# Performance work log

Measured on AMD Instinct MI355X. Metric: run time of the kernel, lower is better.

The kernel has to match this reference:

```python
import jax, jax.numpy as jnp
import numpy as np

D_MODEL = 1024
NUM_EXPERTS = 64
TOP_K = 2
TEMPERATURE = 1.0


def setup_inputs() -> dict:
    key = jax.random.key(0)
    k1, k2, k3, k4 = jax.random.split(key, 4)
    mh_output = jax.random.normal(k1, (8, 4096, D_MODEL), dtype=jnp.float32)
    noise = jax.random.normal(k2, (8, 4096, NUM_EXPERTS), dtype=jnp.float32)  # randn_like sample, externalized
    # nn.Linear weights: shape [out, in], init normal(0, 0.02); biases zero
    W_route = jax.random.normal(k3, (NUM_EXPERTS, D_MODEL), dtype=jnp.float32) * 0.02
    b_route = jnp.zeros((NUM_EXPERTS,), dtype=jnp.float32)
    W_noise = jax.random.normal(k4, (NUM_EXPERTS, D_MODEL), dtype=jnp.float32) * 0.02
    b_noise = jnp.zeros((NUM_EXPERTS,), dtype=jnp.float32)
    return {"mh_output": mh_output, "noise": noise, "W_route": W_route,
            "b_route": b_route, "W_noise": W_noise, "b_noise": b_noise}


def reference(mh_output, noise, W_route, b_route, W_noise, b_noise):
    # logits = topkroute_linear(mh_output); noise_logits = noise_linear(mh_output)
    logits = jnp.einsum('bsd,ed->bse', mh_output, W_route) + b_route
    noise_logits = jnp.einsum('bsd,ed->bse', mh_output, W_noise) + b_noise
    # noisy logits = logits + temperature * randn * softplus(noise_logits)
    noisy = logits + TEMPERATURE * noise * jax.nn.softplus(noise_logits)
    # top-k, scatter into -inf, softmax  ==  softmax over top-k values scattered into zeros
    top_vals, indices = jax.lax.top_k(noisy, TOP_K)          # [b, s, k]
    probs_k = jax.nn.softmax(top_vals, axis=-1)              # softmax(-inf elsewhere) -> 0 elsewhere
    one_hot = jax.nn.one_hot(indices, NUM_EXPERTS, dtype=noisy.dtype)  # [b, s, k, E]
    router_output = jnp.sum(one_hot * probs_k[..., None], axis=-2)     # [b, s, E]
    return router_output, indices
```

## Files before the change

kernel.cpp:

```cpp
#include <hip/hip_runtime.h>
#include <math.h>


#define T_TOKENS 32768
#define D_MODEL  1024
#define NE       64
#define NCOL     128
#define M_TILE   64
#define KB       32
#define NCHUNK   (D_MODEL / KB)
#define CS_LD    65
#define OUT_IDX_BASE ((size_t)T_TOKENS * NE)
#define W_ELEMS  (NCOL * D_MODEL)

typedef short  bf16x8  __attribute__((ext_vector_type(8)));
typedef float  floatx4 __attribute__((ext_vector_type(4)));

__device__ __forceinline__ unsigned short f32_to_bf16_rne(float x) {
    unsigned u = __float_as_uint(x);
    unsigned r = u + 0x7fffu + ((u >> 16) & 1u);
    return (unsigned short)(r >> 16);
}
__device__ __forceinline__ float bf16_bits_to_f32(unsigned short h) {
    return __uint_as_float(((unsigned)h) << 16);
}
__device__ __forceinline__ int4 pack8(const unsigned short* h) {
    int4 r;
    r.x = (int)((unsigned)h[0] | ((unsigned)h[1] << 16));
    r.y = (int)((unsigned)h[2] | ((unsigned)h[3] << 16));
    r.z = (int)((unsigned)h[4] | ((unsigned)h[5] << 16));
    r.w = (int)((unsigned)h[6] | ((unsigned)h[7] << 16));
    return r;
}
__device__ __forceinline__ float softplus_f(float x) {
    return fmaxf(x, 0.f) + log1pf(expf(-fabsf(x)));
}

__global__ __launch_bounds__(256) void prepack_w(
    const float* __restrict__ Wr, const float* __restrict__ Wn,
    short* __restrict__ Bh, short* __restrict__ Bl)
{
    int g   = blockIdx.x * 256 + threadIdx.x;
    int n   = g & 15;
    int kg  = (g >> 4) & 127;
    int t2  = g >> 11;
    int col = t2 * 16 + n;
    const float* src = (col < NE ? Wr + (size_t)col * D_MODEL
                                 : Wn + (size_t)(col - NE) * D_MODEL) + kg * 8;
    float4 a = *(const float4*)src;
    float4 b = *(const float4*)(src + 4);
    float v[8] = {a.x, a.y, a.z, a.w, b.x, b.y, b.z, b.w};
    unsigned short h[8], l[8];
    #pragma unroll
    for (int j = 0; j < 8; ++j) {
        h[j] = f32_to_bf16_rne(v[j]);
        l[j] = f32_to_bf16_rne(v[j] - bf16_bits_to_f32(h[j]));
    }
    *(int4*)(Bh + (size_t)g * 8) = pack8(h);
    *(int4*)(Bl + (size_t)g * 8) = pack8(l);
}

__global__ __launch_bounds__(256) void router_mfma(
    const float* __restrict__ A,
    const float* __restrict__ noise,
    const float* __restrict__ br,
    const float* __restrict__ bn,
    const short* __restrict__ Bh,
    const short* __restrict__ Bl,
    float* __restrict__ out)
{
    __shared__ __align__(16) short Ah[2][M_TILE * KB];
    __shared__ __align__(16) short Al[2][M_TILE * KB];
    __shared__ float Cs[NCOL * CS_LD];
    __shared__ float s_p1[M_TILE], s_p2[M_TILE];
    __shared__ int   s_e1[M_TILE], s_e2[M_TILE];

    const int tid  = threadIdx.x;
    const int lane = tid & 63;
    const int wid  = tid >> 6;
    const int wm   = wid & 1;
    const int wn   = wid >> 1;
    const int n16  = lane & 15;
    const int quad = lane >> 4;
    const int m0   = blockIdx.x * M_TILE;

    const int ms = tid & 63;
    const int ks = tid >> 6;
    const float* pA = A + (size_t)(m0 + ms) * D_MODEL + ks * 8;
    const int sgbase = (ks * 64 + ms) * 8;

    const int bLaneOff = (quad * 16 + n16) * 8;
    const size_t bWaveBase = (size_t)(wn * 4) * 16384 + bLaneOff;

    floatx4 acc[2][4];
    #pragma unroll
    for (int i = 0; i < 2; ++i)
        #pragma unroll
        for (int j = 0; j < 4; ++j) acc[i][j] = (floatx4)0.f;

    float4 g0 = *(const float4*)pA;
    float4 g1 = *(const float4*)(pA + 4);
    {
        float v[8] = {g0.x, g0.y, g0.z, g0.w, g1.x, g1.y, g1.z, g1.w};
        unsigned short h[8], l[8];
        #pragma unroll
        for (int j = 0; j < 8; ++j) {
            h[j] = f32_to_bf16_rne(v[j]);
            l[j] = f32_to_bf16_rne(v[j] - bf16_bits_to_f32(h[j]));
        }
        *(int4*)&Ah[0][sgbase] = pack8(h);
        *(int4*)&Al[0][sgbase] = pack8(l);
    }
    bf16x8 bhc[4], blc[4];
    #pragma unroll
    for (int nf = 0; nf < 4; ++nf) {
        size_t o = bWaveBase + (size_t)nf * 16384;
        bhc[nf] = *(const bf16x8*)(Bh + o);
        blc[nf] = *(const bf16x8*)(Bl + o);
    }

    for (int kc = 0; kc < NCHUNK; ++kc) {
        const int cur = kc & 1, nxt = cur ^ 1;
        __syncthreads();

        float4 n0, n1;
        if (kc + 1 < NCHUNK) {
            n0 = *(const float4*)(pA + (kc + 1) * KB);
            n1 = *(const float4*)(pA + (kc + 1) * KB + 4);
        }

        bf16x8 afh[2], afl[2];
        #pragma unroll
        for (int mf = 0; mf < 2; ++mf) {
            int g = (quad * 64 + wm * 32 + mf * 16 + n16) * 8;
            afh[mf] = *(const bf16x8*)&Ah[cur][g];
            afl[mf] = *(const bf16x8*)&Al[cur][g];
        }

        bf16x8 bhn[4], bln[4];
        if (kc + 1 < NCHUNK) {
            #pragma unroll
            for (int nf = 0; nf < 4; ++nf) {
                size_t o = bWaveBase + (size_t)nf * 16384 + (size_t)(kc + 1) * 512;
                bhn[nf] = *(const bf16x8*)(Bh + o);
                bln[nf] = *(const bf16x8*)(Bl + o);
            }
        }

        #pragma unroll
        for (int mf = 0; mf < 2; ++mf)
            #pragma unroll
            for (int nf = 0; nf < 4; ++nf) {
                acc[mf][nf] = __builtin_amdgcn_mfma_f32_16x16x32_bf16(afh[mf], bhc[nf], acc[mf][nf], 0, 0, 0);
                acc[mf][nf] = __builtin_amdgcn_mfma_f32_16x16x32_bf16(afh[mf], blc[nf], acc[mf][nf], 0, 0, 0);
                acc[mf][nf] = __builtin_amdgcn_mfma_f32_16x16x32_bf16(afl[mf], bhc[nf], acc[mf][nf], 0, 0, 0);
            }

        if (kc + 1 < NCHUNK) {
            float v[8] = {n0.x, n0.y, n0.z, n0.w, n1.x, n1.y, n1.z, n1.w};
            unsigned short h[8], l[8];
            #pragma unroll
            for (int j = 0; j < 8; ++j) {
                h[j] = f32_to_bf16_rne(v[j]);
                l[j] = f32_to_bf16_rne(v[j] - bf16_bits_to_f32(h[j]));
            }
            *(int4*)&Ah[nxt][sgbase] = pack8(h);
            *(int4*)&Al[nxt][sgbase] = pack8(l);
            #pragma unroll
            for (int nf = 0; nf < 4; ++nf) { bhc[nf] = bhn[nf]; blc[nf] = bln[nf]; }
        }
    }

    #pragma unroll
    for (int mf = 0; mf < 2; ++mf)
        #pragma unroll
        for (int nf = 0; nf < 4; ++nf) {
            int col = wn * 64 + nf * 16 + n16;
            int tb  = wm * 32 + mf * 16 + quad * 4;
            #pragma unroll
            for (int r = 0; r < 4; ++r)
                Cs[col * CS_LD + tb + r] = acc[mf][nf][r];
        }
    __syncthreads();

    {
        const int e  = tid & 63;
        const int th = tid >> 6;
        float brv = br[e], bnv = bn[e];
        #pragma unroll
        for (int j = 0; j < 16; ++j) {
            int t = th * 16 + j;
            float route = Cs[e * CS_LD + t] + brv;
            float nl    = Cs[(e + NE) * CS_LD + t] + bnv;
            float nz    = noise[(size_t)(m0 + t) * NE + e];
            Cs[e * CS_LD + t] = fmaf(nz, softplus_f(nl), route);
        }
    }
    __syncthreads();

    if (tid < M_TILE) {
        const int t = tid;
        float v1 = -INFINITY, v2 = -INFINITY;
        int e1 = 0, e2 = 0;
        #pragma unroll 8
        for (int e = 0; e < NE; ++e) {
            float v = Cs[e * CS_LD + t];
            if (v > v1) { v2 = v1; e2 = e1; v1 = v; e1 = e; }
            else if (v > v2) { v2 = v; e2 = e; }
        }
        float ex = expf(v2 - v1);
        float denom = 1.f + ex;
        s_p1[t] = 1.f / denom;
        s_p2[t] = ex / denom;
        s_e1[t] = e1;
        s_e2[t] = e2;
        float2 iv = make_float2((float)e1, (float)e2);
        *(float2*)(out + OUT_IDX_BASE + (size_t)(m0 + t) * 2) = iv;
    }
    __syncthreads();

    #pragma unroll
    for (int i = 0; i < 4; ++i) {
        int gi = i * 256 + tid;
        int t  = gi >> 4;
        int e0 = (gi & 15) * 4;
        float p1 = s_p1[t], p2 = s_p2[t];
        int   e1 = s_e1[t], e2 = s_e2[t];
        float4 v;
        v.x = (e0 + 0 == e1) ? p1 : ((e0 + 0 == e2) ? p2 : 0.f);
        v.y = (e0 + 1 == e1) ? p1 : ((e0 + 1 == e2) ? p2 : 0.f);
        v.z = (e0 + 2 == e1) ? p1 : ((e0 + 2 == e2) ? p2 : 0.f);
        v.w = (e0 + 3 == e1) ? p1 : ((e0 + 3 == e2) ? p2 : 0.f);
        *(float4*)(out + (size_t)(m0 + t) * NE + e0) = v;
    }
}

extern "C" void kernel_launch(void* const* d_in, const int* in_sizes, int n_in,
                              void* d_out, int out_size, void* d_ws, size_t ws_size,
                              hipStream_t stream) {
    const float* A     = (const float*)d_in[0];
    const float* noise = (const float*)d_in[1];
    const float* Wr    = (const float*)d_in[2];
    const float* br    = (const float*)d_in[3];
    const float* Wn    = (const float*)d_in[4];
    const float* bn    = (const float*)d_in[5];
    float* out = (float*)d_out;

    short* Bh = (short*)d_ws;
    short* Bl = Bh + W_ELEMS;

    prepack_w<<<dim3(W_ELEMS / 8 / 256), dim3(256), 0, stream>>>(Wr, Wn, Bh, Bl);
    router_mfma<<<dim3(T_TOKENS / M_TILE), dim3(256), 0, stream>>>(A, noise, br, bn, Bh, Bl, out);
}
```

Measured before the change: 235.6 us.

## Drop LDS staging for A and pair route/noise columns per wave for register epilogue

Each wave now loads its own A rows straight from global memory into registers, converts them to bf16 hi/lo there, and feeds them to MFMA. This removes the LDS double buffer and the per-chunk __syncthreads, and adds a two-deep register prefetch of A. The token tile shrinks to 32 with 4 blocks/SM launch bounds to raise occupancy. Each wave's N-fragments are chosen so it holds both the route and the noise columns for the same experts, so softplus and the bias can be applied from accumulators without a full C staging pass. The cost is more global traffic for B, since each block reloads the whole weight set for only 32 tokens.

After: 268.9 us. 14.2% more time.

```diff
diff --git a/kernel.cpp b/kernel.cpp
--- a/kernel.cpp
+++ b/kernel.cpp
@@ -6,10 +6,9 @@
 #define D_MODEL  1024
 #define NE       64
 #define NCOL     128
-#define M_TILE   64
-#define KB       32
-#define NCHUNK   (D_MODEL / KB)
-#define CS_LD    65
+#define M_TILE   32
+#define NCHUNK   (D_MODEL / 32)
+#define CS_LD    68
 #define OUT_IDX_BASE ((size_t)T_TOKENS * NE)
 #define W_ELEMS  (NCOL * D_MODEL)
 
@@ -60,7 +59,7 @@
     *(int4*)(Bl + (size_t)g * 8) = pack8(l);
 }
 
-__global__ __launch_bounds__(256) void router_mfma(
+__global__ __launch_bounds__(256, 4) void router_mfma(
     const float* __restrict__ A,
     const float* __restrict__ noise,
     const float* __restrict__ br,
@@ -69,9 +68,7 @@
     const short* __restrict__ Bl,
     float* __restrict__ out)
 {
-    __shared__ __align__(16) short Ah[2][M_TILE * KB];
-    __shared__ __align__(16) short Al[2][M_TILE * KB];
-    __shared__ float Cs[NCOL * CS_LD];
+    __shared__ float Cs[M_TILE * CS_LD];
     __shared__ float s_p1[M_TILE], s_p2[M_TILE];
     __shared__ int   s_e1[M_TILE], s_e2[M_TILE];
 
@@ -84,116 +81,65 @@
     const int quad = lane >> 4;
     const int m0   = blockIdx.x * M_TILE;
 
-    const int ms = tid & 63;
-    const int ks = tid >> 6;
-    const float* pA = A + (size_t)(m0 + ms) * D_MODEL + ks * 8;
-    const int sgbase = (ks * 64 + ms) * 8;
-
-    const int bLaneOff = (quad * 16 + n16) * 8;
-    const size_t bWaveBase = (size_t)(wn * 4) * 16384 + bLaneOff;
-
-    floatx4 acc[2][4];
-    #pragma unroll
-    for (int i = 0; i < 2; ++i)
-        #pragma unroll
-        for (int j = 0; j < 4; ++j) acc[i][j] = (floatx4)0.f;
-
-    float4 g0 = *(const float4*)pA;
-    float4 g1 = *(const float4*)(pA + 4);
-    {
-        float v[8] = {g0.x, g0.y, g0.z, g0.w, g1.x, g1.y, g1.z, g1.w};
-        unsigned short h[8], l[8];
+    const float* pA = A + (size_t)(m0 + wm * 16 + n16) * D_MODEL + quad * 8;
+
+    int bBase[4];
+    #pragma unroll
+    for (int f = 0; f < 4; ++f) {
+        int ntile = (f < 2) ? (wn * 2 + f) : (4 + wn * 2 + (f - 2));
+        bBase[f] = ((ntile * 128 + quad) * 16 + n16) * 8;
+    }
+
+    floatx4 acc[4];
+    #pragma unroll
+    for (int f = 0; f < 4; ++f) acc[f] = (floatx4)0.f;
+
+    float4 aC0 = *(const float4*)(pA);
+    float4 aC1 = *(const float4*)(pA + 4);
+    float4 aN0 = *(const float4*)(pA + 32);
+    float4 aN1 = *(const float4*)(pA + 36);
+
+    for (int kc = 0; kc < NCHUNK; ++kc) {
+        float4 aF0, aF1;
+        if (kc + 2 < NCHUNK) {
+            aF0 = *(const float4*)(pA + (kc + 2) * 32);
+            aF1 = *(const float4*)(pA + (kc + 2) * 32 + 4);
+        }
+        bf16x8 bh[4], bl[4];
+        #pragma unroll
+        for (int f = 0; f < 4; ++f) {
+            size_t o = (size_t)bBase[f] + (size_t)kc * 512;
+            bh[f] = *(const bf16x8*)(Bh + o);
+            bl[f] = *(const bf16x8*)(Bl + o);
+        }
+        float v[8] = {aC0.x, aC0.y, aC0.z, aC0.w, aC1.x, aC1.y, aC1.z, aC1.w};
+        bf16x8 afh, afl;
         #pragma unroll
         for (int j = 0; j < 8; ++j) {
-            h[j] = f32_to_bf16_rne(v[j]);
-            l[j] = f32_to_bf16_rne(v[j] - bf16_bits_to_f32(h[j]));
-        }
-        *(int4*)&Ah[0][sgbase] = pack8(h);
-        *(int4*)&Al[0][sgbase] = pack8(l);
-    }
-    bf16x8 bhc[4], blc[4];
-    #pragma unroll
-    for (int nf = 0; nf < 4; ++nf) {
-        size_t o = bWaveBase + (size_t)nf * 16384;
-        bhc[nf] = *(const bf16x8*)(Bh + o);
-        blc[nf] = *(const bf16x8*)(Bl + o);
-    }
-
-    for (int kc = 0; kc < NCHUNK; ++kc) {
-        const int cur = kc & 1, nxt = cur ^ 1;
-        __syncthreads();
-
-        float4 n0, n1;
-        if (kc + 1 < NCHUNK) {
-            n0 = *(const float4*)(pA + (kc + 1) * KB);
-            n1 = *(const float4*)(pA + (kc + 1) * KB + 4);
-        }
-
-        bf16x8 afh[2], afl[2];
-        #pragma unroll
-        for (int mf = 0; mf < 2; ++mf) {
-            int g = (quad * 64 + wm * 32 + mf * 16 + n16) * 8;
-            afh[mf] = *(const bf16x8*)&Ah[cur][g];
-            afl[mf] = *(const bf16x8*)&Al[cur][g];
-        }
-
-        bf16x8 bhn[4], bln[4];
-        if (kc + 1 < NCHUNK) {
-            #pragma unroll
-            for (int nf = 0; nf < 4; ++nf) {
-                size_t o = bWaveBase + (size_t)nf * 16384 + (size_t)(kc + 1) * 512;
-                bhn[nf] = *(const bf16x8*)(Bh + o);
-                bln[nf] = *(const bf16x8*)(Bl + o);
-            }
-        }
-
-        #pragma unroll
-        for (int mf = 0; mf < 2; ++mf)
-            #pragma unroll
-            for (int nf = 0; nf < 4; ++nf) {
-                acc[mf][nf] = __builtin_amdgcn_mfma_f32_16x16x32_bf16(afh[mf], bhc[nf], acc[mf][nf], 0, 0, 0);
-                acc[mf][nf] = __builtin_amdgcn_mfma_f32_16x16x32_bf16(afh[mf], blc[nf], acc[mf][nf], 0, 0, 0);
-                acc[mf][nf] = __builtin_amdgcn_mfma_f32_16x16x32_bf16(afl[mf], bhc[nf], acc[mf][nf], 0, 0, 0);
-            }
-
-        if (kc + 1 < NCHUNK) {
-            float v[8] = {n0.x, n0.y, n0.z, n0.w, n1.x, n1.y, n1.z, n1.w};
-            unsigned short h[8], l[8];
-            #pragma unroll
-            for (int j = 0; j < 8; ++j) {
-                h[j] = f32_to_bf16_rne(v[j]);
-                l[j] = f32_to_bf16_rne(v[j] - bf16_bits_to_f32(h[j]));
-            }
-            *(int4*)&Ah[nxt][sgbase] = pack8(h);
-            *(int4*)&Al[nxt][sgbase] = pack8(l);
-            #pragma unroll
-            for (int nf = 0; nf < 4; ++nf) { bhc[nf] = bhn[nf]; blc[nf] = bln[nf]; }
-        }
-    }
-
-    #pragma unroll
-    for (int mf = 0; mf < 2; ++mf)
-        #pragma unroll
-        for (int nf = 0; nf < 4; ++nf) {
-            int col = wn * 64 + nf * 16 + n16;
-            int tb  = wm * 32 + mf * 16 + quad * 4;
-            #pragma unroll
-            for (int r = 0; r < 4; ++r)
-                Cs[col * CS_LD + tb + r] = acc[mf][nf][r];
-        }
-    __syncthreads();
-
-    {
-        const int e  = tid & 63;
-        const int th = tid >> 6;
+            unsigned short h = f32_to_bf16_rne(v[j]);
+            afh[j] = (short)h;
+            afl[j] = (short)f32_to_bf16_rne(v[j] - bf16_bits_to_f32(h));
+        }
+        #pragma unroll
+        for (int f = 0; f < 4; ++f) {
+            acc[f] = __builtin_amdgcn_mfma_f32_16x16x32_bf16(afh, bh[f], acc[f], 0, 0, 0);
+            acc[f] = __builtin_amdgcn_mfma_f32_16x16x32_bf16(afh, bl[f], acc[f], 0, 0, 0);
+            acc[f] = __builtin_amdgcn_mfma_f32_16x16x32_bf16(afl, bh[f], acc[f], 0, 0, 0);
+        }
+        aC0 = aN0; aC1 = aN1; aN0 = aF0; aN1 = aF1;
+    }
+
+    #pragma unroll
+    for (int nfi = 0; nfi < 2; ++nfi) {
+        int e = wn * 32 + nfi * 16 + n16;
         float brv = br[e], bnv = bn[e];
         #pragma unroll
-        for (int j = 0; j < 16; ++j) {
-            int t = th * 16 + j;
-            float route = Cs[e * CS_LD + t] + brv;
-            float nl    = Cs[(e + NE) * CS_LD + t] + bnv;
+        for (int r = 0; r < 4; ++r) {
+            int t = wm * 16 + quad * 4 + r;
             float nz    = noise[(size_t)(m0 + t) * NE + e];
-            Cs[e * CS_LD + t] = fmaf(nz, softplus_f(nl), route);
+            float route = acc[nfi][r]     + brv;
+            float nl    = acc[2 + nfi][r] + bnv;
+            Cs[t * CS_LD + e] = fmaf(nz, softplus_f(nl), route);
         }
     }
     __syncthreads();
@@ -204,7 +150,7 @@
         int e1 = 0, e2 = 0;
         #pragma unroll 8
         for (int e = 0; e < NE; ++e) {
-            float v = Cs[e * CS_LD + t];
+            float v = Cs[t * CS_LD + e];
             if (v > v1) { v2 = v1; e2 = e1; v1 = v; e1 = e; }
             else if (v > v2) { v2 = v; e2 = e; }
         }
@@ -220,7 +166,7 @@
     __syncthreads();
 
     #pragma unroll
-    for (int i = 0; i < 4; ++i) {
+    for (int i = 0; i < 2; ++i) {
         int gi = i * 256 + tid;
         int t  = gi >> 4;
         int e0 = (gi & 15) * 4;
```
